# Performance work log

Measured on AMD Instinct MI355X. Metric: run time of the kernel, lower is better.

## Reference

```python
import jax, jax.numpy as jnp
import numpy as np

NUM_EXPERTS = 16
TOP_K = 2


def setup_inputs() -> dict:
    key = jax.random.key(0)
    k1, k2, k3 = jax.random.split(key, 3)
    T, H, V = 2048, 2048, 32000
    hidden_states = jax.random.normal(k1, (T, H), dtype=jnp.float32)
    gate_w = jax.random.normal(k2, (NUM_EXPERTS, H), dtype=jnp.float32) * 0.02
    expert_biases = jax.random.normal(k3, (NUM_EXPERTS, V), dtype=jnp.float32) * 0.02
    return {"hidden_states": hidden_states, "gate_w": gate_w, "expert_biases": expert_biases}


def reference(hidden_states, gate_w, expert_biases):
    # gate logits: (T, E)
    gate_logits = jnp.einsum("th,eh->te", hidden_states, gate_w)
    gate_scores = jax.nn.softmax(gate_logits, axis=-1)
    topk_scores, topk_indices = jax.lax.top_k(gate_scores, TOP_K)  # (T, K)
    topk_scores = topk_scores / jnp.sum(topk_scores, axis=-1, keepdims=True)
    # gather expert bias rows: (T, K, V), then weighted sum over K -> (T, V)
    gathered = jnp.take(expert_biases, topk_indices, axis=0)
    bias = jnp.einsum("tk,tkv->tv", topk_scores, gathered)
    # load-balancing aux loss
    expert_usage = jnp.mean(gate_scores, axis=0)  # (E,)
    aux_loss = jnp.sum(expert_usage * jnp.log(expert_usage)) * NUM_EXPERTS
    return bias, aux_loss
```

## Files before the change

### kernel.cpp

```cpp
#include <hip/hip_runtime.h>
#include <math.h>

#define T_TOK 2048
#define H_DIM 2048
#define V_DIM 32000
#define NE    16

typedef float fvec4 __attribute__((ext_vector_type(4)));

#define WS_SCORES(ws)  ((float*)(ws))
#define WS_PARAMS(ws)  ((float4*)((char*)(ws) + NE * T_TOK * sizeof(float)))

__global__ __launch_bounds__(256) void gate_kernel(const float4* __restrict__ hs,
                                                   const float4* __restrict__ gw,
                                                   float* __restrict__ scores,
                                                   float4* __restrict__ params)
{
    const int t   = blockIdx.x;
    const int tid = threadIdx.x;
    const int H4  = H_DIM / 4;

    float acc[NE];
#pragma unroll
    for (int e = 0; e < NE; ++e) acc[e] = 0.f;

    const float4* hrow = hs + (size_t)t * H4;
#pragma unroll
    for (int i = tid; i < H4; i += 256) {
        float4 x = hrow[i];
#pragma unroll
        for (int e = 0; e < NE; ++e) {
            float4 g = gw[e * H4 + i];
            acc[e] += x.x * g.x + x.y * g.y + x.z * g.z + x.w * g.w;
        }
    }

#pragma unroll
    for (int e = 0; e < NE; ++e) {
        float v = acc[e];
#pragma unroll
        for (int off = 32; off > 0; off >>= 1) v += __shfl_down(v, off, 64);
        acc[e] = v;
    }

    __shared__ float partial[4][NE];
    __shared__ float exps[NE + 1];

    const int wave = tid >> 6, lane = tid & 63;
    if (lane == 0) {
#pragma unroll
        for (int e = 0; e < NE; ++e) partial[wave][e] = acc[e];
    }
    __syncthreads();

    if (tid == 0) {
        float logits[NE];
        float m = -INFINITY;
#pragma unroll
        for (int e = 0; e < NE; ++e) {
            logits[e] = partial[0][e] + partial[1][e] + partial[2][e] + partial[3][e];
            m = fmaxf(m, logits[e]);
        }
        float Z = 0.f;
#pragma unroll
        for (int e = 0; e < NE; ++e) { float ex = expf(logits[e] - m); exps[e] = ex; Z += ex; }
        exps[NE] = Z;

        int i0 = 0; float l0 = logits[0];
#pragma unroll
        for (int e = 1; e < NE; ++e) if (logits[e] > l0) { l0 = logits[e]; i0 = e; }
        int i1 = -1; float l1 = -INFINITY;
#pragma unroll
        for (int e = 0; e < NE; ++e) if (e != i0 && logits[e] > l1) { l1 = logits[e]; i1 = e; }

        float e0 = exps[i0], e1 = exps[i1];
        float inv = 1.f / (e0 + e1);
        params[t] = make_float4(e0 * inv, e1 * inv, __int_as_float(i0), __int_as_float(i1));
    }
    __syncthreads();

    if (tid < NE)
        scores[tid * T_TOK + t] = exps[tid] / exps[NE];
}

__global__ __launch_bounds__(256) void bias_kernel(const float4* __restrict__ eb,
                                                   const float4* __restrict__ params,
                                                   float4* __restrict__ out)
{
    const int V4 = V_DIM / 4;
    unsigned int n = blockIdx.x * 256u + threadIdx.x;
    int t = (int)(n / (unsigned)V4);
    int v = (int)(n % (unsigned)V4);

    float4 p = params[t];
    int i0 = __float_as_int(p.z), i1 = __float_as_int(p.w);

    float4 a = eb[(size_t)i0 * V4 + v];
    float4 b = eb[(size_t)i1 * V4 + v];
    fvec4 r;
    r.x = p.x * a.x + p.y * b.x;
    r.y = p.x * a.y + p.y * b.y;
    r.z = p.x * a.z + p.y * b.z;
    r.w = p.x * a.w + p.y * b.w;
    __builtin_nontemporal_store(r, (fvec4*)out + n);
}

__global__ __launch_bounds__(1024) void aux_kernel(const float* __restrict__ scores,
                                                   float* __restrict__ out)
{
    const int e    = threadIdx.x >> 6;
    const int lane = threadIdx.x & 63;

    float s = 0.f;
    const float* row = scores + e * T_TOK;
#pragma unroll
    for (int i = lane; i < T_TOK; i += 64) s += row[i];
#pragma unroll
    for (int off = 32; off > 0; off >>= 1) s += __shfl_down(s, off, 64);

    __shared__ float u[NE];
    if (lane == 0) u[e] = s;
    __syncthreads();

    if (threadIdx.x == 0) {
        float aux = 0.f;
#pragma unroll
        for (int i = 0; i < NE; ++i) {
            float ui = u[i] / (float)T_TOK;
            aux += ui * logf(ui);
        }
        out[0] = aux * (float)NE;
    }
}

extern "C" void kernel_launch(void* const* d_in, const int* in_sizes, int n_in,
                              void* d_out, int out_size, void* d_ws, size_t ws_size,
                              hipStream_t stream)
{
    const float* hs = (const float*)d_in[0];
    const float* gw = (const float*)d_in[1];
    const float* eb = (const float*)d_in[2];
    float* out = (float*)d_out;

    float*  scores = WS_SCORES(d_ws);
    float4* params = WS_PARAMS(d_ws);

    gate_kernel<<<T_TOK, 256, 0, stream>>>((const float4*)hs, (const float4*)gw,
                                           scores, params);

    const unsigned total4 = (unsigned)T_TOK * (V_DIM / 4);
    bias_kernel<<<total4 / 256, 256, 0, stream>>>((const float4*)eb, params, (float4*)out);

    aux_kernel<<<1, 1024, 0, stream>>>(scores, out + (size_t)T_TOK * V_DIM);
}
```

Measured before the change: 293.1 us.

## Fuse gate and bias kernels into one per-token kernel

Result: slower. 316.6 us (+8.0%).

```diff
diff --git a/kernel.cpp b/kernel.cpp
--- a/kernel.cpp
+++ b/kernel.cpp
@@ -9,16 +9,17 @@
 typedef float fvec4 __attribute__((ext_vector_type(4)));
 
 #define WS_SCORES(ws)  ((float*)(ws))
-#define WS_PARAMS(ws)  ((float4*)((char*)(ws) + NE * T_TOK * sizeof(float)))
 
-__global__ __launch_bounds__(256) void gate_kernel(const float4* __restrict__ hs,
-                                                   const float4* __restrict__ gw,
-                                                   float* __restrict__ scores,
-                                                   float4* __restrict__ params)
+__global__ __launch_bounds__(256) void fused_kernel(const float4* __restrict__ hs,
+                                                    const float4* __restrict__ gw,
+                                                    const float4* __restrict__ eb,
+                                                    float* __restrict__ scores,
+                                                    float4* __restrict__ out)
 {
     const int t   = blockIdx.x;
     const int tid = threadIdx.x;
     const int H4  = H_DIM / 4;
+    const int V4  = V_DIM / 4;
 
     float acc[NE];
 #pragma unroll
@@ -44,7 +45,9 @@
     }
 
     __shared__ float partial[4][NE];
-    __shared__ float exps[NE + 1];
+    __shared__ float probs[NE];
+    __shared__ float wsel[2];
+    __shared__ int   isel[2];
 
     const int wave = tid >> 6, lane = tid & 63;
     if (lane == 0) {
@@ -61,10 +64,13 @@
             logits[e] = partial[0][e] + partial[1][e] + partial[2][e] + partial[3][e];
             m = fmaxf(m, logits[e]);
         }
+        float ex[NE];
         float Z = 0.f;
 #pragma unroll
-        for (int e = 0; e < NE; ++e) { float ex = expf(logits[e] - m); exps[e] = ex; Z += ex; }
-        exps[NE] = Z;
+        for (int e = 0; e < NE; ++e) { ex[e] = expf(logits[e] - m); Z += ex[e]; }
+        float invZ = 1.f / Z;
+#pragma unroll
+        for (int e = 0; e < NE; ++e) probs[e] = ex[e] * invZ;
 
         int i0 = 0; float l0 = logits[0];
 #pragma unroll
@@ -73,36 +79,32 @@
 #pragma unroll
         for (int e = 0; e < NE; ++e) if (e != i0 && logits[e] > l1) { l1 = logits[e]; i1 = e; }
 
-        float e0 = exps[i0], e1 = exps[i1];
+        float e0 = ex[i0], e1 = ex[i1];
         float inv = 1.f / (e0 + e1);
-        params[t] = make_float4(e0 * inv, e1 * inv, __int_as_float(i0), __int_as_float(i1));
+        wsel[0] = e0 * inv; wsel[1] = e1 * inv;
+        isel[0] = i0; isel[1] = i1;
     }
     __syncthreads();
 
     if (tid < NE)
-        scores[tid * T_TOK + t] = exps[tid] / exps[NE];
-}
+        scores[tid * T_TOK + t] = probs[tid];
 
-__global__ __launch_bounds__(256) void bias_kernel(const float4* __restrict__ eb,
-                                                   const float4* __restrict__ params,
-                                                   float4* __restrict__ out)
-{
-    const int V4 = V_DIM / 4;
-    unsigned int n = blockIdx.x * 256u + threadIdx.x;
-    int t = (int)(n / (unsigned)V4);
-    int v = (int)(n % (unsigned)V4);
+    const float  w0 = wsel[0], w1 = wsel[1];
+    const float4* r0 = eb + (size_t)isel[0] * V4;
+    const float4* r1 = eb + (size_t)isel[1] * V4;
+    float4* orow = out + (size_t)t * V4;
 
-    float4 p = params[t];
-    int i0 = __float_as_int(p.z), i1 = __float_as_int(p.w);
-
-    float4 a = eb[(size_t)i0 * V4 + v];
-    float4 b = eb[(size_t)i1 * V4 + v];
-    fvec4 r;
-    r.x = p.x * a.x + p.y * b.x;
-    r.y = p.x * a.y + p.y * b.y;
-    r.z = p.x * a.z + p.y * b.z;
-    r.w = p.x * a.w + p.y * b.w;
-    __builtin_nontemporal_store(r, (fvec4*)out + n);
+#pragma unroll 4
+    for (int v = tid; v < V4; v += 256) {
+        float4 a = r0[v];
+        float4 b = r1[v];
+        fvec4 r;
+        r.x = w0 * a.x + w1 * b.x;
+        r.y = w0 * a.y + w1 * b.y;
+        r.z = w0 * a.z + w1 * b.z;
+        r.w = w0 * a.w + w1 * b.w;
+        __builtin_nontemporal_store(r, (fvec4*)orow + v);
+    }
 }
 
 __global__ __launch_bounds__(1024) void aux_kernel(const float* __restrict__ scores,
@@ -142,14 +144,10 @@
     const float* eb = (const float*)d_in[2];
     float* out = (float*)d_out;
 
-    float*  scores = WS_SCORES(d_ws);
-    float4* params = WS_PARAMS(d_ws);
+    float* scores = WS_SCORES(d_ws);
 
-    gate_kernel<<<T_TOK, 256, 0, stream>>>((const float4*)hs, (const float4*)gw,
-                                           scores, params);
-
-    const unsigned total4 = (unsigned)T_TOK * (V_DIM / 4);
-    bias_kernel<<<total4 / 256, 256, 0, stream>>>((const float4*)eb, params, (float4*)out);
+    fused_kernel<<<T_TOK, 256, 0, stream>>>((const float4*)hs, (const float4*)gw,
+                                            (const float4*)eb, scores, (float4*)out);
 
     aux_kernel<<<1, 1024, 0, stream>>>(scores, out + (size_t)T_TOK * V_DIM);
 }
```
